# Optimization experiments

Hardware: AMD Instinct MI355X
Metric: run time of the kernel (lower is better)

## Reference

```python
import jax, jax.numpy as jnp
import numpy as np
from jax import lax

E4M3 = jnp.float8_e4m3fn
DIM_NUMS = (((1,), (0,)), ((), ()))  # contract inputs last dim with kernel first dim


def quantize_dequantize(x, q_dtype, scale, compute_dtype):
    dtype_max = jnp.finfo(q_dtype).max.astype(compute_dtype)
    s = scale.astype(compute_dtype)
    scaled = x.astype(compute_dtype) / s
    clipped = jnp.clip(scaled, -dtype_max, dtype_max)
    qx = clipped.astype(q_dtype)
    # dequantize back to x.dtype
    return qx.astype(x.dtype) * scale.astype(x.dtype)


def setup_inputs() -> dict:
    key = jax.random.key(0)
    k1, k2 = jax.random.split(key)
    H = 1024  # amax_history_length
    return {
        "inputs": jax.random.normal(k1, (8192, 4096), dtype=jnp.float32),
        "kernel": jax.random.normal(k2, (4096, 4096), dtype=jnp.float32),
        "input_scale": jnp.ones((1,), jnp.float32),
        "input_amax_history": jnp.zeros((H,), jnp.float32),
        "kernel_scale": jnp.ones((1,), jnp.float32),
        "kernel_amax_history": jnp.zeros((H,), jnp.float32),
        "output_grad_scale": jnp.ones((1,), jnp.float32),
        "output_grad_amax_history": jnp.zeros((H,), jnp.float32),
    }


def reference(inputs, kernel, input_scale, input_amax_history, kernel_scale,
              kernel_amax_history, output_grad_scale, output_grad_amax_history):
    comp_dtype = kernel.dtype
    inputs = jnp.asarray(inputs, comp_dtype)
    # in_qdq on both operands (e4m3); out_qdq is identity in the forward pass.
    lhs_qdq = quantize_dequantize(inputs, E4M3, input_scale, comp_dtype)
    rhs_qdq = quantize_dequantize(kernel, E4M3, kernel_scale, comp_dtype)
    out = lax.dot_general(lhs_qdq, rhs_qdq, DIM_NUMS, precision=None)
    return out
```

## Files before the change

### kernel.cpp

```cpp
#include <hip/hip_runtime.h>
#include <stdint.h>

#define M_DIM 8192
#define N_DIM 4096
#define K_DIM 4096
#define NT (K_DIM / 128)

typedef float f32x4 __attribute__((ext_vector_type(4)));
typedef int v4i __attribute__((ext_vector_type(4)));
typedef int v8i __attribute__((ext_vector_type(8)));
typedef uint32_t u32;


__device__ __forceinline__ void gload_lds16(const void* g, void* l) {
  __builtin_amdgcn_global_load_lds(
      (__attribute__((address_space(1))) void*)(g),
      (__attribute__((address_space(3))) void*)(l), 16, 0, 0);
}

__device__ __forceinline__ float clipdiv(float v, float s) {
  v = v / s;
  return fminf(fmaxf(v, -448.f), 448.f);
}

__device__ __forceinline__ u32 pack4_fp8(float a, float b, float c, float d) {
  int w = __builtin_amdgcn_cvt_pk_fp8_f32(a, b, 0, false);
  w = __builtin_amdgcn_cvt_pk_fp8_f32(c, d, w, true);
  return (u32)w;
}

__device__ __forceinline__ v8i rd8(const void* lo, const void* hi) {
  v4i l = *(const v4i*)lo;
  v4i h = *(const v4i*)hi;
  return __builtin_shufflevector(l, h, 0, 1, 2, 3, 4, 5, 6, 7);
}

__device__ __forceinline__ f32x4 mfma8(v8i a, v8i b, f32x4 c) {
  return __builtin_amdgcn_mfma_scale_f32_16x16x128_f8f6f4(
      a, b, c, 0, 0, 0, 0x7f7f7f7f, 0, 0x7f7f7f7f);
}


__global__ __launch_bounds__(256) void quant_a(const float* __restrict__ x,
                                               u32* __restrict__ q,
                                               const float* __restrict__ scale,
                                               int nv4) {
  int base = blockIdx.x * 1024 + threadIdx.x;
  float s = scale[0];
#pragma unroll
  for (int r = 0; r < 4; ++r) {
    int idx = base + r * 256;
    if (idx < nv4) {
      float4 v = ((const float4*)x)[idx];
      q[idx] = pack4_fp8(clipdiv(v.x, s), clipdiv(v.y, s),
                         clipdiv(v.z, s), clipdiv(v.w, s));
    }
  }
}


__global__ __launch_bounds__(256) void quant_b_t(const float* __restrict__ B,
                                                 uint8_t* __restrict__ qT,
                                                 const float* __restrict__ scale) {
  __shared__ __align__(16) uint8_t lt[64 * 80];
  int tid = threadIdx.x;
  int kt = blockIdx.x * 64;
  int nt = blockIdx.y * 64;
  float s = scale[0];

  int kl = tid >> 4;
  int n4 = (tid & 15) * 4;
#pragma unroll
  for (int rep = 0; rep < 4; ++rep) {
    int k = kl + rep * 16;
    float4 v = *(const float4*)&B[(long)(kt + k) * N_DIM + nt + n4];
    u32 w = pack4_fp8(clipdiv(v.x, s), clipdiv(v.y, s),
                      clipdiv(v.z, s), clipdiv(v.w, s));
    lt[(n4 + 0) * 80 + k] = (uint8_t)(w & 0xff);
    lt[(n4 + 1) * 80 + k] = (uint8_t)((w >> 8) & 0xff);
    lt[(n4 + 2) * 80 + k] = (uint8_t)((w >> 16) & 0xff);
    lt[(n4 + 3) * 80 + k] = (uint8_t)(w >> 24);
  }
  __syncthreads();
  int n = tid >> 2, ch = tid & 3;
  uint4 o = *(const uint4*)&lt[n * 80 + ch * 16];
  *(uint4*)&qT[(long)(nt + n) * K_DIM + kt + ch * 16] = o;
}


template <int BUF>
__device__ __forceinline__ void compute_tile(const uint8_t* lds,
                                             const int (&offA)[4][2],
                                             const int (&offB)[4][2],
                                             f32x4 (&acc)[4][4]) {
  const uint8_t* Ab = lds + BUF * 32768;
  const uint8_t* Bb = lds + BUF * 32768 + 16384;
  v8i a[4], b[4];
#pragma unroll
  for (int i = 0; i < 4; ++i) a[i] = rd8(Ab + offA[i][0], Ab + offA[i][1]);
#pragma unroll
  for (int j = 0; j < 4; ++j) b[j] = rd8(Bb + offB[j][0], Bb + offB[j][1]);
#pragma unroll
  for (int i = 0; i < 4; ++i)
#pragma unroll
    for (int j = 0; j < 4; ++j) acc[i][j] = mfma8(a[i], b[j], acc[i][j]);
}

template <int BUF>
__device__ __forceinline__ void stage_tile(const uint8_t* const (&gA)[4],
                                           const uint8_t* const (&gB)[4],
                                           uint8_t* lds, const int (&ldo)[4],
                                           long ko) {
#pragma unroll
  for (int r = 0; r < 4; ++r)
    gload_lds16(gA[r] + ko, lds + BUF * 32768 + ldo[r]);
#pragma unroll
  for (int r = 0; r < 4; ++r)
    gload_lds16(gB[r] + ko, lds + BUF * 32768 + 16384 + ldo[r]);
}

__global__ __launch_bounds__(256) void gemm_mx(const uint8_t* __restrict__ Aq,
                                               const uint8_t* __restrict__ BqT,
                                               float* __restrict__ C,
                                               const float* __restrict__ sA,
                                               const float* __restrict__ sB) {
  __shared__ __align__(16) uint8_t lds[65536];

  const int tid = threadIdx.x;
  const int lane = tid & 63;
  const int w = tid >> 6;
  const int wr = w >> 1, wc = w & 1;
  const long bm = (long)blockIdx.y * 128;
  const long bn = (long)blockIdx.x * 128;

  float s = sA[0] * sB[0];
  asm volatile("" ::"v"(s));

  const uint8_t* gA[4];
  const uint8_t* gB[4];
  int ldo[4];
#pragma unroll
  for (int r = 0; r < 4; ++r) {
    int gid = tid + 256 * r;
    int row = gid >> 3, gc = gid & 7;
    int sc = (gc ^ (row & 7)) << 4;
    gA[r] = Aq + (bm + row) * (long)K_DIM + sc;
    gB[r] = BqT + (bn + row) * (long)K_DIM + sc;
    ldo[r] = gid * 16;
  }

  const int r16 = lane & 15;
  const int hi = lane >> 4;
  int offA[4][2], offB[4][2];
#pragma unroll
  for (int i = 0; i < 4; ++i) {
    int ra = wr * 64 + i * 16 + r16;
    int rb = wc * 64 + i * 16 + r16;
#pragma unroll
    for (int g = 0; g < 2; ++g) {
      int lg = 2 * hi + g;
      offA[i][g] = ra * 128 + ((lg ^ (ra & 7)) << 4);
      offB[i][g] = rb * 128 + ((lg ^ (rb & 7)) << 4);
    }
  }

  f32x4 acc[4][4] = {};

  stage_tile<0>(gA, gB, lds, ldo, 0);
  asm volatile("s_waitcnt vmcnt(0)" ::: "memory");
  __builtin_amdgcn_s_barrier();

  for (int i = 0; i < NT / 2; ++i) {
    long ko1 = (long)((2 * i + 1) & (NT - 1)) * 128;
    stage_tile<1>(gA, gB, lds, ldo, ko1);
    compute_tile<0>(lds, offA, offB, acc);
    asm volatile("s_waitcnt vmcnt(0)" ::: "memory");
    __builtin_amdgcn_s_barrier();

    long ko2 = (long)((2 * i + 2) & (NT - 1)) * 128;
    stage_tile<0>(gA, gB, lds, ldo, ko2);
    compute_tile<1>(lds, offA, offB, acc);
    asm volatile("s_waitcnt vmcnt(0)" ::: "memory");
    __builtin_amdgcn_s_barrier();
  }

#pragma unroll
  for (int i = 0; i < 4; ++i)
#pragma unroll
    for (int j = 0; j < 4; ++j) {
      long row = bm + wr * 64 + i * 16 + hi * 4;
      long col = bn + wc * 64 + j * 16 + r16;
      float* cp = C + row * N_DIM + col;
#pragma unroll
      for (int q = 0; q < 4; ++q) cp[(long)q * N_DIM] = acc[i][j][q] * s;
    }
}


extern "C" void kernel_launch(void* const* d_in, const int* in_sizes, int n_in,
                              void* d_out, int out_size, void* d_ws, size_t ws_size,
                              hipStream_t stream) {
  const float* A = (const float*)d_in[0];
  const float* B = (const float*)d_in[1];
  const float* sA = (const float*)d_in[2];
  const float* sB = (const float*)d_in[4];
  float* out = (float*)d_out;

  uint8_t* Aq = (uint8_t*)d_ws;
  uint8_t* BqT = Aq + (size_t)M_DIM * K_DIM;

  int nv4_a = M_DIM * K_DIM / 4;
  quant_a<<<nv4_a / 1024, 256, 0, stream>>>(A, (u32*)Aq, sA, nv4_a);
  quant_b_t<<<dim3(K_DIM / 64, N_DIM / 64), 256, 0, stream>>>(B, BqT, sB);
  gemm_mx<<<dim3(N_DIM / 128, M_DIM / 128), 256, 0, stream>>>(Aq, BqT, out, sA, sB);
}
```

Measured before the change: 202.4 us.

## Enlarge GEMM tile to 256x256 with 8 waves, XCD-aware block swizzle, word-wise B transpose

The GEMM block tile grows from 128x128 to 256x256, with 512 threads in a 2x4 wave grid where each wave computes 128x64. LDS use doubles to 128KB for double-buffered A and B. Blocks are remapped to a 1D grid with a swizzle that groups neighbouring tiles on the same XCD, to improve L2 reuse. The B quantize-transpose kernel now packs four k values into one u32 and stores whole words into padded LDS, replacing byte-wise scattered stores. The cost is more accumulator registers per wave and fewer resident blocks per CU because of the 128KB LDS.

```diff
diff --git a/kernel.cpp b/kernel.cpp
--- a/kernel.cpp
+++ b/kernel.cpp
@@ -62,49 +62,40 @@
 __global__ __launch_bounds__(256) void quant_b_t(const float* __restrict__ B,
                                                  uint8_t* __restrict__ qT,
                                                  const float* __restrict__ scale) {
-  __shared__ __align__(16) uint8_t lt[64 * 80];
+  __shared__ u32 lt[64 * 17];
   int tid = threadIdx.x;
   int kt = blockIdx.x * 64;
   int nt = blockIdx.y * 64;
   float s = scale[0];
 
-  int kl = tid >> 4;
-  int n4 = (tid & 15) * 4;
-#pragma unroll
-  for (int rep = 0; rep < 4; ++rep) {
-    int k = kl + rep * 16;
-    float4 v = *(const float4*)&B[(long)(kt + k) * N_DIM + nt + n4];
-    u32 w = pack4_fp8(clipdiv(v.x, s), clipdiv(v.y, s),
-                      clipdiv(v.z, s), clipdiv(v.w, s));
-    lt[(n4 + 0) * 80 + k] = (uint8_t)(w & 0xff);
-    lt[(n4 + 1) * 80 + k] = (uint8_t)((w >> 8) & 0xff);
-    lt[(n4 + 2) * 80 + k] = (uint8_t)((w >> 16) & 0xff);
-    lt[(n4 + 3) * 80 + k] = (uint8_t)(w >> 24);
-  }
+  int kq = tid >> 4;
+  int nq = tid & 15;
+  int k0 = kq * 4, n0 = nq * 4;
+  const float* src = B + (long)(kt + k0) * N_DIM + nt + n0;
+  float4 v0 = *(const float4*)(src);
+  float4 v1 = *(const float4*)(src + N_DIM);
+  float4 v2 = *(const float4*)(src + 2 * N_DIM);
+  float4 v3 = *(const float4*)(src + 3 * N_DIM);
+
+  lt[(n0 + 0) * 17 + kq] = pack4_fp8(clipdiv(v0.x, s), clipdiv(v1.x, s),
+                                     clipdiv(v2.x, s), clipdiv(v3.x, s));
+  lt[(n0 + 1) * 17 + kq] = pack4_fp8(clipdiv(v0.y, s), clipdiv(v1.y, s),
+                                     clipdiv(v2.y, s), clipdiv(v3.y, s));
+  lt[(n0 + 2) * 17 + kq] = pack4_fp8(clipdiv(v0.z, s), clipdiv(v1.z, s),
+                                     clipdiv(v2.z, s), clipdiv(v3.z, s));
+  lt[(n0 + 3) * 17 + kq] = pack4_fp8(clipdiv(v0.w, s), clipdiv(v1.w, s),
+                                     clipdiv(v2.w, s), clipdiv(v3.w, s));
   __syncthreads();
+
   int n = tid >> 2, ch = tid & 3;
-  uint4 o = *(const uint4*)&lt[n * 80 + ch * 16];
+  uint4 o;
+  o.x = lt[n * 17 + ch * 4 + 0];
+  o.y = lt[n * 17 + ch * 4 + 1];
+  o.z = lt[n * 17 + ch * 4 + 2];
+  o.w = lt[n * 17 + ch * 4 + 3];
   *(uint4*)&qT[(long)(nt + n) * K_DIM + kt + ch * 16] = o;
 }
 
-
-template <int BUF>
-__device__ __forceinline__ void compute_tile(const uint8_t* lds,
-                                             const int (&offA)[4][2],
-                                             const int (&offB)[4][2],
-                                             f32x4 (&acc)[4][4]) {
-  const uint8_t* Ab = lds + BUF * 32768;
-  const uint8_t* Bb = lds + BUF * 32768 + 16384;
-  v8i a[4], b[4];
-#pragma unroll
-  for (int i = 0; i < 4; ++i) a[i] = rd8(Ab + offA[i][0], Ab + offA[i][1]);
-#pragma unroll
-  for (int j = 0; j < 4; ++j) b[j] = rd8(Bb + offB[j][0], Bb + offB[j][1]);
-#pragma unroll
-  for (int i = 0; i < 4; ++i)
-#pragma unroll
-    for (int j = 0; j < 4; ++j) acc[i][j] = mfma8(a[i], b[j], acc[i][j]);
-}
 
 template <int BUF>
 __device__ __forceinline__ void stage_tile(const uint8_t* const (&gA)[4],
@@ -116,22 +107,52 @@
     gload_lds16(gA[r] + ko, lds + BUF * 32768 + ldo[r]);
 #pragma unroll
   for (int r = 0; r < 4; ++r)
-    gload_lds16(gB[r] + ko, lds + BUF * 32768 + 16384 + ldo[r]);
-}
-
-__global__ __launch_bounds__(256) void gemm_mx(const uint8_t* __restrict__ Aq,
-                                               const uint8_t* __restrict__ BqT,
-                                               float* __restrict__ C,
-                                               const float* __restrict__ sA,
-                                               const float* __restrict__ sB) {
-  __shared__ __align__(16) uint8_t lds[65536];
+    gload_lds16(gB[r] + ko, lds + 65536 + BUF * 32768 + ldo[r]);
+}
+
+template <int BUF>
+__device__ __forceinline__ void compute_tile(const uint8_t* lds,
+                                             const int (&offA)[8][2],
+                                             const int (&offB)[4][2],
+                                             f32x4 (&acc)[8][4]) {
+  const uint8_t* Ab = lds + BUF * 32768;
+  const uint8_t* Bb = lds + 65536 + BUF * 32768;
+  v8i b[4];
+#pragma unroll
+  for (int j = 0; j < 4; ++j) b[j] = rd8(Bb + offB[j][0], Bb + offB[j][1]);
+#pragma unroll
+  for (int h = 0; h < 2; ++h) {
+    v8i a[4];
+#pragma unroll
+    for (int i = 0; i < 4; ++i)
+      a[i] = rd8(Ab + offA[h * 4 + i][0], Ab + offA[h * 4 + i][1]);
+#pragma unroll
+    for (int i = 0; i < 4; ++i)
+#pragma unroll
+      for (int j = 0; j < 4; ++j)
+        acc[h * 4 + i][j] = mfma8(a[i], b[j], acc[h * 4 + i][j]);
+  }
+}
+
+__global__ __launch_bounds__(512, 2) void gemm_mx(const uint8_t* __restrict__ Aq,
+                                                  const uint8_t* __restrict__ BqT,
+                                                  float* __restrict__ C,
+                                                  const float* __restrict__ sA,
+                                                  const float* __restrict__ sB) {
+  __shared__ __align__(16) uint8_t lds[131072];
 
   const int tid = threadIdx.x;
   const int lane = tid & 63;
-  const int w = tid >> 6;
-  const int wr = w >> 1, wc = w & 1;
-  const long bm = (long)blockIdx.y * 128;
-  const long bn = (long)blockIdx.x * 128;
+  const int wid = tid >> 6;
+  const int wr = wid >> 2;
+  const int wc = wid & 3;
+  const int r16 = lane & 15;
+  const int hi = lane >> 4;
+
+  int bid = blockIdx.x;
+  int wg = (bid & 7) * 64 + (bid >> 3);
+  const long bm = (long)(wg >> 4) * 256;
+  const long bn = (long)(wg & 15) * 256;
 
   float s = sA[0] * sB[0];
   asm volatile("" ::"v"(s));
@@ -141,7 +162,7 @@
   int ldo[4];
 #pragma unroll
   for (int r = 0; r < 4; ++r) {
-    int gid = tid + 256 * r;
+    int gid = tid + 512 * r;
     int row = gid >> 3, gc = gid & 7;
     int sc = (gc ^ (row & 7)) << 4;
     gA[r] = Aq + (bm + row) * (long)K_DIM + sc;
@@ -149,22 +170,27 @@
     ldo[r] = gid * 16;
   }
 
-  const int r16 = lane & 15;
-  const int hi = lane >> 4;
-  int offA[4][2], offB[4][2];
-#pragma unroll
-  for (int i = 0; i < 4; ++i) {
-    int ra = wr * 64 + i * 16 + r16;
-    int rb = wc * 64 + i * 16 + r16;
+  int offA[8][2], offB[4][2];
+#pragma unroll
+  for (int mi = 0; mi < 8; ++mi) {
+    int ra = wr * 128 + mi * 16 + r16;
 #pragma unroll
     for (int g = 0; g < 2; ++g) {
       int lg = 2 * hi + g;
-      offA[i][g] = ra * 128 + ((lg ^ (ra & 7)) << 4);
-      offB[i][g] = rb * 128 + ((lg ^ (rb & 7)) << 4);
-    }
-  }
-
-  f32x4 acc[4][4] = {};
+      offA[mi][g] = ra * 128 + ((lg ^ (ra & 7)) << 4);
+    }
+  }
+#pragma unroll
+  for (int nj = 0; nj < 4; ++nj) {
+    int rb = wc * 64 + nj * 16 + r16;
+#pragma unroll
+    for (int g = 0; g < 2; ++g) {
+      int lg = 2 * hi + g;
+      offB[nj][g] = rb * 128 + ((lg ^ (rb & 7)) << 4);
+    }
+  }
+
+  f32x4 acc[8][4] = {};
 
   stage_tile<0>(gA, gB, lds, ldo, 0);
   asm volatile("s_waitcnt vmcnt(0)" ::: "memory");
@@ -184,15 +210,17 @@
     __builtin_amdgcn_s_barrier();
   }
 
-#pragma unroll
-  for (int i = 0; i < 4; ++i)
-#pragma unroll
-    for (int j = 0; j < 4; ++j) {
-      long row = bm + wr * 64 + i * 16 + hi * 4;
-      long col = bn + wc * 64 + j * 16 + r16;
+  const float sc = s;
+#pragma unroll
+  for (int mi = 0; mi < 8; ++mi)
+#pragma unroll
+    for (int nj = 0; nj < 4; ++nj) {
+      long row = bm + wr * 128 + mi * 16 + hi * 4;
+      long col = bn + wc * 64 + nj * 16 + r16;
       float* cp = C + row * N_DIM + col;
-#pragma unroll
-      for (int q = 0; q < 4; ++q) cp[(long)q * N_DIM] = acc[i][j][q] * s;
+      f32x4 v = acc[mi][nj];
+#pragma unroll
+      for (int q = 0; q < 4; ++q) cp[(long)q * N_DIM] = v[q] * sc;
     }
 }
 
@@ -212,5 +240,5 @@
   int nv4_a = M_DIM * K_DIM / 4;
   quant_a<<<nv4_a / 1024, 256, 0, stream>>>(A, (u32*)Aq, sA, nv4_a);
   quant_b_t<<<dim3(K_DIM / 64, N_DIM / 64), 256, 0, stream>>>(B, BqT, sB);
-  gemm_mx<<<dim3(N_DIM / 128, M_DIM / 128), 256, 0, stream>>>(Aq, BqT, out, sA, sB);
-}
+  gemm_mx<<<dim3((M_DIM / 256) * (N_DIM / 256)), 512, 0, stream>>>(Aq, BqT, out, sA, sB);
+}
```

New measurement: 188.9 us. 6.6% less time.
